# Performance work log

Measured on AMD Instinct MI355X. Metric: run time of the kernel, lower is better.

The kernel has to match this reference:

```python
import jax, jax.numpy as jnp
import numpy as np

N_USERS = 17449
N_ITEMS = 48676
N = N_USERS + N_ITEMS  # 66125 nodes
H = 2    # heads
C = 64   # out_channels per head
D_IN = 64
E = 2_000_000
NEG_SLOPE = 0.2


def setup_inputs() -> dict:
    key = jax.random.key(0)
    ks = jax.random.split(key, 7)
    edge_index = jax.random.randint(ks[0], (2, E), 0, N, dtype=jnp.int32)
    # xavier-normal-ish init for embeddings and GAT params
    users_feature = jax.random.normal(ks[1], (N_USERS, D_IN), dtype=jnp.float32) * 0.1
    items_feature = jax.random.normal(ks[2], (N_ITEMS, D_IN), dtype=jnp.float32) * 0.1
    W = jax.random.normal(ks[3], (D_IN, H * C), dtype=jnp.float32) * (1.0 / np.sqrt(D_IN))
    att_src = jax.random.normal(ks[4], (H, C), dtype=jnp.float32) * 0.1
    att_dst = jax.random.normal(ks[5], (H, C), dtype=jnp.float32) * 0.1
    bias = jnp.zeros((H * C,), dtype=jnp.float32)
    return {
        "edge_index": edge_index,
        "users_feature": users_feature,
        "items_feature": items_feature,
        "W": W,
        "att_src": att_src,
        "att_dst": att_dst,
        "bias": bias,
    }


def reference(edge_index, users_feature, items_feature, W, att_src, att_dst, bias):
    # node features: [N, D_IN]
    x = jnp.concatenate([users_feature, items_feature], axis=0)
    # linear transform -> per-head features [N, H, C]
    h = (x @ W).reshape(N, H, C)
    # per-node attention logits [N, H]
    a_src = jnp.einsum("nhc,hc->nh", h, att_src)
    a_dst = jnp.einsum("nhc,hc->nh", h, att_dst)
    # add self loops (PyG GATConv default)
    loops = jnp.arange(N, dtype=edge_index.dtype)
    src = jnp.concatenate([edge_index[0], loops])
    dst = jnp.concatenate([edge_index[1], loops])
    # per-edge attention score [E+N, H]
    e = jax.nn.leaky_relu(a_src[src] + a_dst[dst], negative_slope=NEG_SLOPE)
    # segment softmax over destination node
    m = jax.lax.stop_gradient(jax.ops.segment_max(e, dst, num_segments=N))
    ex = jnp.exp(e - m[dst])
    denom = jax.ops.segment_sum(ex, dst, num_segments=N)
    alpha = ex / (denom[dst] + 1e-16)
    # scatter-add weighted source features -> [N, H, C]
    out = jax.ops.segment_sum(alpha[:, :, None] * h[src], dst, num_segments=N)
    # concat heads + bias -> [N, H*C]
    return out.reshape(N, H * C) + bias
```

## Files before the change

kernel.cpp:

```cpp
#include <hip/hip_runtime.h>
#include <hip/hip_fp16.h>
#include <math.h>

#define NEG_SLOPE 0.2f
#define BSHIFT 6
#define BNODES 64
#define MAXB 1056
#define CAP 2816
#define BIN_E 2048

typedef unsigned short ushort8_v __attribute__((ext_vector_type(8)));
typedef short  short8_v  __attribute__((ext_vector_type(8)));
typedef float  float4_v  __attribute__((ext_vector_type(4)));

__device__ __forceinline__ unsigned short f2bf(float f) {
    unsigned u = __float_as_uint(f);
    u = (u + 0x7FFFu + ((u >> 16) & 1u)) >> 16;
    return (unsigned short)u;
}
__device__ __forceinline__ float bf2f(unsigned short b) {
    return __uint_as_float(((unsigned)b) << 16);
}
__device__ __forceinline__ float lrelu(float x) {
    return x > 0.f ? x : NEG_SLOPE * x;
}
__device__ __forceinline__ unsigned f2h_bits(float f) {
    __half_raw hr = __half_raw(__float2half_rn(f));
    return (unsigned)hr.x;
}
__device__ __forceinline__ float h2f_bits(unsigned short u) {
    __half_raw hr; hr.x = u;
    return __half2float(__half(hr));
}

__global__ __launch_bounds__(512) void k_xform_bin(
        const float* __restrict__ users,
        const float* __restrict__ items,
        const float* __restrict__ W,
        const float* __restrict__ att_src,
        const float* __restrict__ att_dst,
        unsigned short* __restrict__ hb,
        float* __restrict__ a_src,
        float* __restrict__ a_dst,
        const int* __restrict__ src,
        const int* __restrict__ dst,
        int* __restrict__ tails,
        int* __restrict__ stage_g,
        int nedges, int nbuckets, int n_users, int N,
        int nxf, int ntotal)
{
    __shared__ __align__(16) char smem[128 * 130 * 2];

    const int tid  = threadIdx.x;
    const int lane = tid & 63;
    const int wid  = tid >> 6;

    const int bid = blockIdx.x;
    const long long num = (long long)nxf;
    const int xf_before = (int)(((long long)bid * num) / ntotal);
    const bool is_xf = ((((long long)(bid + 1) * num) / ntotal) > xf_before);

    if (!is_xf) {
        const int bin_id = bid - xf_before;
        int* cnt     = (int*)smem;
        int* runoff  = cnt + MAXB;
        int* cursor  = runoff + MAXB;
        int* runbase = cursor + MAXB;
        int* stage   = runbase + MAXB;
        unsigned short* sb = (unsigned short*)(stage + BIN_E);

        const int base = bin_id * BIN_E;
        const int nvalid = min(BIN_E, nedges - base);

        for (int i = tid; i < nbuckets; i += 512) cnt[i] = 0;
        __syncthreads();

        int myrec[BIN_E / 512];
        int myb[BIN_E / 512];
        #pragma unroll
        for (int k = 0; k < BIN_E / 512; ++k) {
            int i = base + k * 512 + tid;
            if (i < nedges) {
                const int d = dst[i];
                myrec[k] = src[i] | ((d & (BNODES - 1)) << 17);
                myb[k] = d >> BSHIFT;
                atomicAdd(&cnt[myb[k]], 1);
            } else {
                myb[k] = -1;
            }
        }
        __syncthreads();

        if (wid == 0) {
            int running = 0;
            for (int b2 = 0; b2 < nbuckets; b2 += 64) {
                int idx = b2 + lane;
                int v = (idx < nbuckets) ? cnt[idx] : 0;
                int incl = v;
                #pragma unroll
                for (int off = 1; off < 64; off <<= 1) {
                    int t = __shfl_up(incl, off);
                    if (lane >= off) incl += t;
                }
                if (idx < nbuckets) runoff[idx] = running + incl - v;
                running += __shfl(incl, 63);
            }
        }
        __syncthreads();

        for (int i = tid; i < nbuckets; i += 512) cursor[i] = runoff[i];
        __syncthreads();

        #pragma unroll
        for (int k = 0; k < BIN_E / 512; ++k) {
            if (myb[k] >= 0) {
                int pos = atomicAdd(&cursor[myb[k]], 1);
                stage[pos] = myrec[k];
                sb[pos] = (unsigned short)myb[k];
            }
        }

        for (int i = tid; i < nbuckets; i += 512)
            if (cnt[i] > 0) runbase[i] = atomicAdd(&tails[i], cnt[i]);
        __syncthreads();

        for (int i = tid; i < nvalid; i += 512) {
            const int b = sb[i];
            const int idx = runbase[b] + (i - runoff[b]);
            if (idx < CAP)
                stage_g[(size_t)b * CAP + idx] = stage[i];
        }
        return;
    }

    unsigned short (*tile)[130] = (unsigned short (*)[130])smem;
    const int blk  = xf_before;
    const int quad = lane >> 4;
    const int l16  = lane & 15;
    const int tb   = blk * 128 + wid * 16;

    short8_v bfrag[8][2];
    #pragma unroll
    for (int t = 0; t < 8; ++t)
        #pragma unroll
        for (int h2 = 0; h2 < 2; ++h2)
            #pragma unroll
            for (int j = 0; j < 8; ++j)
                bfrag[t][h2][j] = (short)f2bf(
                    W[(h2 * 32 + quad * 8 + j) * 128 + t * 16 + l16]);

    float atts[8], attd[8];
    #pragma unroll
    for (int t = 0; t < 8; ++t) {
        atts[t] = att_src[t * 16 + l16];
        attd[t] = att_dst[t * 16 + l16];
    }

    const int arow = tb + l16;
    short8_v a0 = (short8_v)0, a1 = (short8_v)0;
    if (arow < N) {
        const float* xr = (arow < n_users)
            ? (users + (size_t)arow * 64)
            : (items + (size_t)(arow - n_users) * 64);
        const float4_v x0 = *reinterpret_cast<const float4_v*>(xr + quad * 8);
        const float4_v x1 = *reinterpret_cast<const float4_v*>(xr + quad * 8 + 4);
        const float4_v x2 = *reinterpret_cast<const float4_v*>(xr + 32 + quad * 8);
        const float4_v x3 = *reinterpret_cast<const float4_v*>(xr + 32 + quad * 8 + 4);
        #pragma unroll
        for (int j = 0; j < 4; ++j) {
            a0[j]     = (short)f2bf(x0[j]);
            a0[j + 4] = (short)f2bf(x1[j]);
            a1[j]     = (short)f2bf(x2[j]);
            a1[j + 4] = (short)f2bf(x3[j]);
        }
    }

    float4_v acc[8];
    #pragma unroll
    for (int t = 0; t < 8; ++t) {
        acc[t] = (float4_v)0.f;
        acc[t] = __builtin_amdgcn_mfma_f32_16x16x32_bf16(a0, bfrag[t][0], acc[t], 0, 0, 0);
        acc[t] = __builtin_amdgcn_mfma_f32_16x16x32_bf16(a1, bfrag[t][1], acc[t], 0, 0, 0);
    }

    const int wrow0 = tb + quad * 4;
    float s0[4] = {0,0,0,0}, s1[4] = {0,0,0,0};
    float d0[4] = {0,0,0,0}, d1[4] = {0,0,0,0};
    #pragma unroll
    for (int t = 0; t < 8; ++t) {
        #pragma unroll
        for (int r = 0; r < 4; ++r) {
            const float v = acc[t][r];
            if (t < 4) { s0[r] = fmaf(v, atts[t], s0[r]);
                         d0[r] = fmaf(v, attd[t], d0[r]); }
            else       { s1[r] = fmaf(v, atts[t], s1[r]);
                         d1[r] = fmaf(v, attd[t], d1[r]); }
            tile[wid * 16 + quad * 4 + r][t * 16 + l16] = f2bf(v);
        }
    }

    #pragma unroll
    for (int off = 1; off < 16; off <<= 1) {
        #pragma unroll
        for (int r = 0; r < 4; ++r) {
            s0[r] += __shfl_xor(s0[r], off);
            s1[r] += __shfl_xor(s1[r], off);
            d0[r] += __shfl_xor(d0[r], off);
            d1[r] += __shfl_xor(d1[r], off);
        }
    }
    if (l16 == 0) {
        #pragma unroll
        for (int r = 0; r < 4; ++r) {
            const int row = wrow0 + r;
            if (row < N) {
                a_src[row * 2]     = s0[r];
                a_src[row * 2 + 1] = s1[r];
                a_dst[row * 2]     = d0[r];
                a_dst[row * 2 + 1] = d1[r];
            }
        }
    }

    __syncthreads();
    const int base_node = blk * 128;
    const int nrem = min(128, N - base_node);
    for (int k = tid; k < nrem * 16; k += 512) {
        const int n = k >> 4, g = k & 15;
        ushort8_v v;
        #pragma unroll
        for (int j = 0; j < 8; ++j) v[j] = tile[n][g * 8 + j];
        *reinterpret_cast<ushort8_v*>(
            hb + (size_t)(base_node + n) * 128 + g * 8) = v;
    }
}

__global__ __launch_bounds__(512) void k_sort_gather(
        const int* __restrict__ stage_g,
        const int* __restrict__ tails,
        const float* __restrict__ a_src,
        const float* __restrict__ a_dst,
        const unsigned short* __restrict__ hb,
        const float* __restrict__ bias,
        float* __restrict__ out,
        int N)
{
    __shared__ int cnt[BNODES];
    __shared__ int off[BNODES];
    __shared__ int cursor[BNODES];
    __shared__ float adst[BNODES][2];
    __shared__ int lin[CAP];
    __shared__ int2 lsorted[CAP];

    const int b    = blockIdx.x;
    const int tid  = threadIdx.x;
    const int lane = tid & 63;
    const int wid  = tid >> 6;
    const int node0  = b << BSHIFT;
    const int nnodes = min(BNODES, N - node0);
    const int nrec = min(tails[b], CAP);
    const int* bucket = stage_g + (size_t)b * CAP;

    if (tid < BNODES) {
        cnt[tid] = 0;
        if (tid < nnodes) {
            const float2 ad = *reinterpret_cast<const float2*>(
                a_dst + 2 * (node0 + tid));
            adst[tid][0] = ad.x;
            adst[tid][1] = ad.y;
        } else {
            adst[tid][0] = adst[tid][1] = 0.f;
        }
    }
    __syncthreads();

    for (int i = tid; i < nrec; i += 512) {
        const int r = bucket[i];
        lin[i] = r;
        atomicAdd(&cnt[(r >> 17) & (BNODES - 1)], 1);
    }
    __syncthreads();

    if (wid == 0) {
        const int v = cnt[lane];
        int incl = v;
        #pragma unroll
        for (int o = 1; o < 64; o <<= 1) {
            int t = __shfl_up(incl, o);
            if (lane >= o) incl += t;
        }
        off[lane] = incl - v;
        cursor[lane] = incl - v;
    }
    __syncthreads();

    for (int i = tid; i < nrec; i += 512) {
        const int r = lin[i];
        const int s = r & 0x1FFFF;
        const int n = (r >> 17) & (BNODES - 1);
        const float2 as2 = *reinterpret_cast<const float2*>(a_src + 2 * s);
        const unsigned e0 = f2h_bits(__expf(lrelu(as2.x + adst[n][0])));
        const unsigned e1 = f2h_bits(__expf(lrelu(as2.y + adst[n][1])));
        const int pos = atomicAdd(&cursor[n], 1);
        if (pos < CAP) {
            int2 rec;
            rec.x = (int)((e1 << 16) | e0);
            rec.y = s;
            lsorted[pos] = rec;
        }
    }
    __syncthreads();

    const int q  = lane >> 4;
    const int sl = lane & 15;
    const int hd = sl >> 3;

    for (int n = wid; n < nnodes; n += 8) {
        const int d = node0 + n;
        const float2 as2 = *reinterpret_cast<const float2*>(a_src + 2 * d);
        const float exs0 = __expf(lrelu(as2.x + adst[n][0]));
        const float exs1 = __expf(lrelu(as2.y + adst[n][1]));
        const int start = off[n];
        const int cnt1  = cnt[n] + 1;

        float acc[8];
        #pragma unroll
        for (int i = 0; i < 8; ++i) acc[i] = 0.f;
        float den = 0.f;

        #pragma unroll 4
        for (int v = q; v < cnt1; v += 4) {
            int s; float ex;
            if (v == 0) {
                s = d;  ex = hd ? exs1 : exs0;
            } else {
                const int2 r = lsorted[start + v - 1];
                s = r.y;
                const unsigned eb = (unsigned)r.x;
                ex = h2f_bits(hd ? (unsigned short)(eb >> 16)
                                 : (unsigned short)(eb & 0xFFFFu));
            }
            const ushort8_v hv = *reinterpret_cast<const ushort8_v*>(
                hb + (size_t)s * 128 + sl * 8);
            den += ex;
            #pragma unroll
            for (int i = 0; i < 8; ++i)
                acc[i] = fmaf(ex, bf2f(hv[i]), acc[i]);
        }

        #pragma unroll
        for (int o = 16; o <= 32; o <<= 1) {
            #pragma unroll
            for (int i = 0; i < 8; ++i) acc[i] += __shfl_xor(acc[i], o);
            den += __shfl_xor(den, o);
        }

        if (q == 0) {
            const float inv = 1.f / (den + 1e-16f);
            float4 o0, o1;
            o0.x = acc[0] * inv + bias[sl * 8 + 0];
            o0.y = acc[1] * inv + bias[sl * 8 + 1];
            o0.z = acc[2] * inv + bias[sl * 8 + 2];
            o0.w = acc[3] * inv + bias[sl * 8 + 3];
            o1.x = acc[4] * inv + bias[sl * 8 + 4];
            o1.y = acc[5] * inv + bias[sl * 8 + 5];
            o1.z = acc[6] * inv + bias[sl * 8 + 6];
            o1.w = acc[7] * inv + bias[sl * 8 + 7];
            float* op = out + (size_t)d * 128 + sl * 8;
            *reinterpret_cast<float4*>(op)     = o0;
            *reinterpret_cast<float4*>(op + 4) = o1;
        }
    }
}

extern "C" void kernel_launch(void* const* d_in, const int* in_sizes, int n_in,
                              void* d_out, int out_size, void* d_ws, size_t ws_size,
                              hipStream_t stream) {
    const int*   edge  = (const int*)  d_in[0];
    const float* users = (const float*)d_in[1];
    const float* items = (const float*)d_in[2];
    const float* W     = (const float*)d_in[3];
    const float* att_s = (const float*)d_in[4];
    const float* att_d = (const float*)d_in[5];
    const float* bias  = (const float*)d_in[6];

    const int E       = in_sizes[0] / 2;
    const int n_users = in_sizes[1] / 64;
    const int n_items = in_sizes[2] / 64;
    const int N       = n_users + n_items;
    const int nbuckets = (N + BNODES - 1) >> BSHIFT;

    float* out = (float*)d_out;

    char* ws = (char*)d_ws;
    unsigned short* hb = (unsigned short*)ws;
    ws += (size_t)N * 128 * sizeof(unsigned short);
    int*   stage    = (int*)ws;    ws += (size_t)MAXB * CAP * sizeof(int);
    float* a_src    = (float*)ws;  ws += (size_t)N * 2 * sizeof(float);
    float* a_dst    = (float*)ws;  ws += (size_t)N * 2 * sizeof(float);
    int*   tails    = (int*)ws;

    const int* src = edge;
    const int* dst = edge + E;

    hipMemsetAsync(tails, 0, MAXB * sizeof(int), stream);

    const int nbin = (E + BIN_E - 1) / BIN_E;
    const int nxf  = (N + 127) / 128;
    const int ntotal = nbin + nxf;
    k_xform_bin<<<ntotal, 512, 0, stream>>>(
        users, items, W, att_s, att_d, hb, a_src, a_dst,
        src, dst, tails, stage, E, nbuckets, n_users, N, nxf, ntotal);

    k_sort_gather<<<nbuckets, 512, 0, stream>>>(
        stage, tails, a_src, a_dst, hb, bias, out, N);
}
```

Before: 237.1 us.

## Sort bucket edges by destination and source range; enlarge binning chunks

The bucket sort in the gather kernel now keys on destination node plus the upper bits of the source index (1024 keys). Edges for each destination come out grouped by source range, which should improve cache locality of the h gathers. The local copy of bucket records in LDS is removed and the records are re-read from global memory instead. The binning pass processes 4096 edges per block, and the runoff array is reused to hold combined offsets, which shrinks that kernel's LDS footprint. The cost is a longer prefix scan over 1024 keys and a second global read of each bucket.

```diff
diff --git a/kernel.cpp b/kernel.cpp
--- a/kernel.cpp
+++ b/kernel.cpp
@@ -7,7 +7,8 @@
 #define BNODES 64
 #define MAXB 1056
 #define CAP 2816
-#define BIN_E 2048
+#define BIN_E 4096
+#define NKEY 1024
 
 typedef unsigned short ushort8_v __attribute__((ext_vector_type(8)));
 typedef short  short8_v  __attribute__((ext_vector_type(8)));
@@ -49,7 +50,7 @@
         int nedges, int nbuckets, int n_users, int N,
         int nxf, int ntotal)
 {
-    __shared__ __align__(16) char smem[128 * 130 * 2];
+    __shared__ __align__(16) char smem[3 * MAXB * 4 + BIN_E * 4 + BIN_E * 2];
 
     const int tid  = threadIdx.x;
     const int lane = tid & 63;
@@ -65,8 +66,7 @@
         int* cnt     = (int*)smem;
         int* runoff  = cnt + MAXB;
         int* cursor  = runoff + MAXB;
-        int* runbase = cursor + MAXB;
-        int* stage   = runbase + MAXB;
+        int* stage   = cursor + MAXB;
         unsigned short* sb = (unsigned short*)(stage + BIN_E);
 
         const int base = bin_id * BIN_E;
@@ -121,12 +121,15 @@
         }
 
         for (int i = tid; i < nbuckets; i += 512)
-            if (cnt[i] > 0) runbase[i] = atomicAdd(&tails[i], cnt[i]);
+            if (cnt[i] > 0) {
+                const int rb = atomicAdd(&tails[i], cnt[i]);
+                runoff[i] = rb - runoff[i];
+            }
         __syncthreads();
 
         for (int i = tid; i < nvalid; i += 512) {
             const int b = sb[i];
-            const int idx = runbase[b] + (i - runoff[b]);
+            const int idx = runoff[b] + i;
             if (idx < CAP)
                 stage_g[(size_t)b * CAP + idx] = stage[i];
         }
@@ -245,11 +248,10 @@
         float* __restrict__ out,
         int N)
 {
-    __shared__ int cnt[BNODES];
-    __shared__ int off[BNODES];
-    __shared__ int cursor[BNODES];
+    __shared__ int cnt[NKEY];
+    __shared__ int off[NKEY + 1];
+    __shared__ int cursor[NKEY];
     __shared__ float adst[BNODES][2];
-    __shared__ int lin[CAP];
     __shared__ int2 lsorted[CAP];
 
     const int b    = blockIdx.x;
@@ -261,8 +263,8 @@
     const int nrec = min(tails[b], CAP);
     const int* bucket = stage_g + (size_t)b * CAP;
 
+    for (int i = tid; i < NKEY; i += 512) cnt[i] = 0;
     if (tid < BNODES) {
-        cnt[tid] = 0;
         if (tid < nnodes) {
             const float2 ad = *reinterpret_cast<const float2*>(
                 a_dst + 2 * (node0 + tid));
@@ -276,32 +278,40 @@
 
     for (int i = tid; i < nrec; i += 512) {
         const int r = bucket[i];
-        lin[i] = r;
-        atomicAdd(&cnt[(r >> 17) & (BNODES - 1)], 1);
+        const int key = (((r >> 17) & (BNODES - 1)) << 4) | ((r & 0x1FFFF) >> 13);
+        atomicAdd(&cnt[key], 1);
     }
     __syncthreads();
 
     if (wid == 0) {
-        const int v = cnt[lane];
-        int incl = v;
-        #pragma unroll
-        for (int o = 1; o < 64; o <<= 1) {
-            int t = __shfl_up(incl, o);
-            if (lane >= o) incl += t;
-        }
-        off[lane] = incl - v;
-        cursor[lane] = incl - v;
-    }
+        int running = 0;
+        #pragma unroll
+        for (int c = 0; c < NKEY; c += 64) {
+            const int v = cnt[c + lane];
+            int incl = v;
+            #pragma unroll
+            for (int o = 1; o < 64; o <<= 1) {
+                int t = __shfl_up(incl, o);
+                if (lane >= o) incl += t;
+            }
+            off[c + lane] = running + incl - v;
+            running += __shfl(incl, 63);
+        }
+        if (lane == 0) off[NKEY] = running;
+    }
+    __syncthreads();
+    for (int i = tid; i < NKEY; i += 512) cursor[i] = off[i];
     __syncthreads();
 
     for (int i = tid; i < nrec; i += 512) {
-        const int r = lin[i];
+        const int r = bucket[i];
         const int s = r & 0x1FFFF;
         const int n = (r >> 17) & (BNODES - 1);
+        const int key = (n << 4) | (s >> 13);
         const float2 as2 = *reinterpret_cast<const float2*>(a_src + 2 * s);
         const unsigned e0 = f2h_bits(__expf(lrelu(as2.x + adst[n][0])));
         const unsigned e1 = f2h_bits(__expf(lrelu(as2.y + adst[n][1])));
-        const int pos = atomicAdd(&cursor[n], 1);
+        const int pos = atomicAdd(&cursor[key], 1);
         if (pos < CAP) {
             int2 rec;
             rec.x = (int)((e1 << 16) | e0);
@@ -320,8 +330,8 @@
         const float2 as2 = *reinterpret_cast<const float2*>(a_src + 2 * d);
         const float exs0 = __expf(lrelu(as2.x + adst[n][0]));
         const float exs1 = __expf(lrelu(as2.y + adst[n][1]));
-        const int start = off[n];
-        const int cnt1  = cnt[n] + 1;
+        const int start = off[n << 4];
+        const int cnt1  = off[(n << 4) + 16] - start + 1;
 
         float acc[8];
         #pragma unroll
```

Result: faster. 228.6 us (-3.6%).

## Hold gather records in registers, halve gather block size, double bin chunk

Applied to the files above, without the earlier changes.

The sort-gather kernel now runs 256-thread blocks and keeps each thread's bucket records in a register array instead of staging them in a shared `lin` buffer. This cuts shared memory per block, which should let more blocks fit per CU. The binning blocks now each handle 4096 edges, so fewer blocks do the global tail atomics. The separate run-base array is folded into `runoff` to save LDS. In exchange, each gather thread holds 11 records in registers and has fewer waves per block to process the 64 nodes, and each bin block does more serial work.

```diff
diff --git a/kernel.cpp b/kernel.cpp
--- a/kernel.cpp
+++ b/kernel.cpp
@@ -7,7 +7,9 @@
 #define BNODES 64
 #define MAXB 1056
 #define CAP 2816
-#define BIN_E 2048
+#define BIN_E 4096
+#define SG_THREADS 256
+#define RPT (CAP / SG_THREADS)
 
 typedef unsigned short ushort8_v __attribute__((ext_vector_type(8)));
 typedef short  short8_v  __attribute__((ext_vector_type(8)));
@@ -49,7 +51,7 @@
         int nedges, int nbuckets, int n_users, int N,
         int nxf, int ntotal)
 {
-    __shared__ __align__(16) char smem[128 * 130 * 2];
+    __shared__ __align__(16) char smem[3 * MAXB * 4 + BIN_E * 4 + BIN_E * 2];
 
     const int tid  = threadIdx.x;
     const int lane = tid & 63;
@@ -65,8 +67,7 @@
         int* cnt     = (int*)smem;
         int* runoff  = cnt + MAXB;
         int* cursor  = runoff + MAXB;
-        int* runbase = cursor + MAXB;
-        int* stage   = runbase + MAXB;
+        int* stage   = cursor + MAXB;
         unsigned short* sb = (unsigned short*)(stage + BIN_E);
 
         const int base = bin_id * BIN_E;
@@ -121,12 +122,15 @@
         }
 
         for (int i = tid; i < nbuckets; i += 512)
-            if (cnt[i] > 0) runbase[i] = atomicAdd(&tails[i], cnt[i]);
+            if (cnt[i] > 0) {
+                const int rb = atomicAdd(&tails[i], cnt[i]);
+                runoff[i] = rb - runoff[i];
+            }
         __syncthreads();
 
         for (int i = tid; i < nvalid; i += 512) {
             const int b = sb[i];
-            const int idx = runbase[b] + (i - runoff[b]);
+            const int idx = runoff[b] + i;
             if (idx < CAP)
                 stage_g[(size_t)b * CAP + idx] = stage[i];
         }
@@ -235,7 +239,7 @@
     }
 }
 
-__global__ __launch_bounds__(512) void k_sort_gather(
+__global__ __launch_bounds__(SG_THREADS) void k_sort_gather(
         const int* __restrict__ stage_g,
         const int* __restrict__ tails,
         const float* __restrict__ a_src,
@@ -249,7 +253,6 @@
     __shared__ int off[BNODES];
     __shared__ int cursor[BNODES];
     __shared__ float adst[BNODES][2];
-    __shared__ int lin[CAP];
     __shared__ int2 lsorted[CAP];
 
     const int b    = blockIdx.x;
@@ -274,10 +277,17 @@
     }
     __syncthreads();
 
-    for (int i = tid; i < nrec; i += 512) {
-        const int r = bucket[i];
-        lin[i] = r;
-        atomicAdd(&cnt[(r >> 17) & (BNODES - 1)], 1);
+    int myrec[RPT];
+    #pragma unroll
+    for (int k = 0; k < RPT; ++k) {
+        const int i = k * SG_THREADS + tid;
+        if (i < nrec) {
+            const int r = bucket[i];
+            myrec[k] = r;
+            atomicAdd(&cnt[(r >> 17) & (BNODES - 1)], 1);
+        } else {
+            myrec[k] = -1;
+        }
     }
     __syncthreads();
 
@@ -294,19 +304,22 @@
     }
     __syncthreads();
 
-    for (int i = tid; i < nrec; i += 512) {
-        const int r = lin[i];
-        const int s = r & 0x1FFFF;
-        const int n = (r >> 17) & (BNODES - 1);
-        const float2 as2 = *reinterpret_cast<const float2*>(a_src + 2 * s);
-        const unsigned e0 = f2h_bits(__expf(lrelu(as2.x + adst[n][0])));
-        const unsigned e1 = f2h_bits(__expf(lrelu(as2.y + adst[n][1])));
-        const int pos = atomicAdd(&cursor[n], 1);
-        if (pos < CAP) {
-            int2 rec;
-            rec.x = (int)((e1 << 16) | e0);
-            rec.y = s;
-            lsorted[pos] = rec;
+    #pragma unroll
+    for (int k = 0; k < RPT; ++k) {
+        const int r = myrec[k];
+        if (r >= 0) {
+            const int s = r & 0x1FFFF;
+            const int n = (r >> 17) & (BNODES - 1);
+            const float2 as2 = *reinterpret_cast<const float2*>(a_src + 2 * s);
+            const unsigned e0 = f2h_bits(__expf(lrelu(as2.x + adst[n][0])));
+            const unsigned e1 = f2h_bits(__expf(lrelu(as2.y + adst[n][1])));
+            const int pos = atomicAdd(&cursor[n], 1);
+            if (pos < CAP) {
+                int2 rec;
+                rec.x = (int)((e1 << 16) | e0);
+                rec.y = s;
+                lsorted[pos] = rec;
+            }
         }
     }
     __syncthreads();
@@ -315,7 +328,7 @@
     const int sl = lane & 15;
     const int hd = sl >> 3;
 
-    for (int n = wid; n < nnodes; n += 8) {
+    for (int n = wid; n < nnodes; n += 4) {
         const int d = node0 + n;
         const float2 as2 = *reinterpret_cast<const float2*>(a_src + 2 * d);
         const float exs0 = __expf(lrelu(as2.x + adst[n][0]));
@@ -412,6 +425,6 @@
         users, items, W, att_s, att_d, hb, a_src, a_dst,
         src, dst, tails, stage, E, nbuckets, n_users, N, nxf, ntotal);
 
-    k_sort_gather<<<nbuckets, 512, 0, stream>>>(
+    k_sort_gather<<<nbuckets, SG_THREADS, 0, stream>>>(
         stage, tails, a_src, a_dst, hb, bias, out, N);
 }
```

After: 210.4 us, median of 2. 1.13x faster.
